# Performance work log

Measured on AMD Instinct MI355X. Metric: run time of the kernel, lower is better.

## Reference

```python
import jax, jax.numpy as jnp
import numpy as np

B, S, D = 2, 1024, 2048
H, KVH, HD = 16, 4, 128
HID, E, K = 4096, 8, 2
EPS = 1e-5
NEG = -1e9  # finite stand-in for -inf in the causal mask


def setup_inputs() -> dict:
    key = jax.random.key(0)
    ks = jax.random.split(key, 16)
    sc = 0.02
    x = jax.random.normal(ks[0], (B, S, D), jnp.float32)
    # rotary tables (theta = 10000), as cos/sin instead of complex
    inv_freq = 1.0 / (10000.0 ** (jnp.arange(0, HD, 2, dtype=jnp.float32) / HD))
    t = jnp.arange(S, dtype=jnp.float32)
    fr = jnp.outer(t, inv_freq)  # [S, HD/2]
    freqs_cos, freqs_sin = jnp.cos(fr), jnp.sin(fr)
    positions = jnp.arange(S, dtype=jnp.int32)
    mask = jnp.where(jnp.tril(jnp.ones((S, S), bool)), 0.0, NEG).astype(jnp.float32)
    attn_norm_w = jnp.ones((D,), jnp.float32)
    ffn_norm_w = jnp.ones((D,), jnp.float32)
    wq = jax.random.normal(ks[1], (D, H * HD), jnp.float32) * sc
    wk = jax.random.normal(ks[2], (D, KVH * HD), jnp.float32) * sc
    wv = jax.random.normal(ks[3], (D, KVH * HD), jnp.float32) * sc
    wo = jax.random.normal(ks[4], (H * HD, D), jnp.float32) * sc
    gate_w = jax.random.normal(ks[5], (D, E), jnp.float32) * sc
    w1 = jax.random.normal(ks[6], (E, D, HID), jnp.float32) * sc
    w2 = jax.random.normal(ks[7], (E, HID, D), jnp.float32) * sc
    w3 = jax.random.normal(ks[8], (E, D, HID), jnp.float32) * sc
    return dict(x=x, freqs_cos=freqs_cos, freqs_sin=freqs_sin, positions=positions,
                mask=mask, attn_norm_w=attn_norm_w, ffn_norm_w=ffn_norm_w,
                wq=wq, wk=wk, wv=wv, wo=wo, gate_w=gate_w, w1=w1, w2=w2, w3=w3)


def rmsnorm(x, w):
    xf = x.astype(jnp.float32)
    n = xf * jax.lax.rsqrt(jnp.mean(xf * xf, axis=-1, keepdims=True) + EPS)
    return n.astype(x.dtype) * w


def rope(t, cos, sin):
    # t: [B,S,nh,HD]; interleaved (real, imag) pairs like torch.view_as_complex
    tr = t.reshape(*t.shape[:-1], HD // 2, 2)
    xr, xi = tr[..., 0], tr[..., 1]
    c = cos[None, :, None, :]
    s = sin[None, :, None, :]
    out = jnp.stack([xr * c - xi * s, xr * s + xi * c], axis=-1)
    return out.reshape(t.shape)


def block_fwd(x, freqs_cos, freqs_sin, mask, attn_norm_w, ffn_norm_w,
              wq, wk, wv, wo, gate_w, w1, w2, w3):
    # ---- attention ----
    h = rmsnorm(x, attn_norm_w)
    q = (h @ wq).reshape(B, S, H, HD)
    k = (h @ wk).reshape(B, S, KVH, HD)
    v = (h @ wv).reshape(B, S, KVH, HD)
    q = rope(q, freqs_cos, freqs_sin)
    k = rope(k, freqs_cos, freqs_sin)
    rep = H // KVH
    k = jnp.repeat(k, rep, axis=2)  # [B,S,H,HD]
    v = jnp.repeat(v, rep, axis=2)
    scale = HD ** -0.5
    scores = jnp.einsum('bqhd,bkhd->bhqk', q, k) * scale + mask[None, None]
    probs = jax.nn.softmax(scores.astype(jnp.float32), axis=-1).astype(q.dtype)
    attn = jnp.einsum('bhqk,bkhd->bqhd', probs, v).reshape(B, S, H * HD)
    h1 = x + attn @ wo
    # ---- MoE FFN ----
    t = rmsnorm(h1, ffn_norm_w).reshape(-1, D)  # [T,D]
    logits = t @ gate_w  # [T,E]
    topw, sel = jax.lax.top_k(logits, K)
    topw = jax.nn.softmax(topw.astype(jnp.float32), axis=-1).astype(t.dtype)
    out = jnp.zeros_like(t)
    for i in range(E):
        coef = jnp.sum(jnp.where(sel == i, topw, 0.0), axis=-1, keepdims=True)  # [T,1]
        ff = (jax.nn.silu(t @ w1[i]) * (t @ w3[i])) @ w2[i]
        out = out + coef * ff
    return h1 + out.reshape(B, S, D)


def reference(x, freqs_cos, freqs_sin, positions, mask, attn_norm_w, ffn_norm_w,
              wq, wk, wv, wo, gate_w, w1, w2, w3):
    # prefill branch (positions.shape[0] > 1): KV-cache scatter is a write-only
    # side effect in the original and does not affect this output.
    del positions
    return block_fwd(x, freqs_cos, freqs_sin, mask, attn_norm_w, ffn_norm_w,
                     wq, wk, wv, wo, gate_w, w1, w2, w3)
```

## Files before the change

### kernel.cpp

```cpp
#include <hip/hip_runtime.h>

typedef unsigned short u16;
typedef unsigned int u32;
typedef __bf16 bf16x8 __attribute__((ext_vector_type(8)));
typedef _Float16 f16;
typedef f16 f16x8 __attribute__((ext_vector_type(8)));
typedef float f32x4 __attribute__((ext_vector_type(4)));

#define DEVFN __device__ __forceinline__

constexpr int kB = 2, kS = 1024, kD = 2048, kH = 16, kKVH = 4, kHD = 128;
constexpr int kHID = 4096, kE = 8;
constexpr int kRows = kB * kS;
constexpr int kQKVN = kH*kHD + 2*kKVH*kHD;
constexpr int kSlotsPad = 5120;
constexpr int kMaxTiles = 40;
constexpr float kEps = 1e-5f;
constexpr float kNeg = -1000000000.0f;
constexpr float kScale = 0.08838834764831845f;

DEVFN u16 f2bf(float f) {
  u32 u = __float_as_uint(f);
  return (u16)((u + 0x7fffu + ((u >> 16) & 1u)) >> 16);
}
DEVFN float bf2f(u16 u) { u32 v = ((u32)u) << 16; return __uint_as_float(v); }

DEVFN void split8v(float4 a, float4 b, f16x8& hi, f16x8& lo) {
  float v[8] = {a.x, a.y, a.z, a.w, b.x, b.y, b.z, b.w};
  #pragma unroll
  for (int e = 0; e < 8; ++e) {
    f16 h = (f16)v[e];
    hi[e] = h;
    lo[e] = (f16)(v[e] - (float)h);
  }
}

DEVFN void gll16(const void* g, void* l) {
  __builtin_amdgcn_global_load_lds(
      (const __attribute__((address_space(1))) void*)g,
      (__attribute__((address_space(3))) void*)l, 16, 0, 0);
}

__global__ __launch_bounds__(256) void rms_split_kernel(const float* __restrict__ in,
    const float* __restrict__ w, f16* __restrict__ oh, f16* __restrict__ ol) {
  int row = blockIdx.x, tid = threadIdx.x;
  const float* x = in + (size_t)row * kD;
  float4 v0 = *(const float4*)&x[tid*8];
  float4 v1 = *(const float4*)&x[tid*8+4];
  float ss = v0.x*v0.x+v0.y*v0.y+v0.z*v0.z+v0.w*v0.w
           + v1.x*v1.x+v1.y*v1.y+v1.z*v1.z+v1.w*v1.w;
  #pragma unroll
  for (int off = 32; off; off >>= 1) ss += __shfl_xor(ss, off);
  __shared__ float red[4];
  if ((tid & 63) == 0) red[tid >> 6] = ss;
  __syncthreads();
  float tot = red[0] + red[1] + red[2] + red[3];
  float rs = rsqrtf(tot * (1.0f/kD) + kEps);
  float4 w0 = *(const float4*)&w[tid*8];
  float4 w1 = *(const float4*)&w[tid*8+4];
  float4 o0, o1;
  o0.x = v0.x*rs*w0.x; o0.y = v0.y*rs*w0.y; o0.z = v0.z*rs*w0.z; o0.w = v0.w*rs*w0.w;
  o1.x = v1.x*rs*w1.x; o1.y = v1.y*rs*w1.y; o1.z = v1.z*rs*w1.z; o1.w = v1.w*rs*w1.w;
  f16x8 hi, lo;
  split8v(o0, o1, hi, lo);
  *(f16x8*)&oh[(size_t)row*kD + tid*8] = hi;
  *(f16x8*)&ol[(size_t)row*kD + tid*8] = lo;
}

__global__ __launch_bounds__(256) void split_kernel(const float* __restrict__ in,
    f16* __restrict__ oh, f16* __restrict__ ol, int n8) {
  int i = blockIdx.x * 256 + threadIdx.x;
  if (i >= n8) return;
  float4 a = *(const float4*)&in[i*8];
  float4 b = *(const float4*)&in[i*8+4];
  f16x8 hi, lo;
  split8v(a, b, hi, lo);
  *(f16x8*)&oh[i*8] = hi;
  *(f16x8*)&ol[i*8] = lo;
}

__global__ __launch_bounds__(256) void rms_bf16_kernel(const float* __restrict__ in,
    const float* __restrict__ w, u16* __restrict__ out) {
  int row = blockIdx.x, tid = threadIdx.x;
  const float* x = in + (size_t)row * kD;
  float4 v0 = *(const float4*)&x[tid*8];
  float4 v1 = *(const float4*)&x[tid*8+4];
  float ss = v0.x*v0.x+v0.y*v0.y+v0.z*v0.z+v0.w*v0.w
           + v1.x*v1.x+v1.y*v1.y+v1.z*v1.z+v1.w*v1.w;
  #pragma unroll
  for (int off = 32; off; off >>= 1) ss += __shfl_xor(ss, off);
  __shared__ float red[4];
  if ((tid & 63) == 0) red[tid >> 6] = ss;
  __syncthreads();
  float tot = red[0] + red[1] + red[2] + red[3];
  float rs = rsqrtf(tot * (1.0f/kD) + kEps);
  float4 w0 = *(const float4*)&w[tid*8];
  float4 w1 = *(const float4*)&w[tid*8+4];
  union { int4 i4; u16 u[8]; } pk;
  pk.u[0] = f2bf(v0.x*rs*w0.x); pk.u[1] = f2bf(v0.y*rs*w0.y);
  pk.u[2] = f2bf(v0.z*rs*w0.z); pk.u[3] = f2bf(v0.w*rs*w0.w);
  pk.u[4] = f2bf(v1.x*rs*w1.x); pk.u[5] = f2bf(v1.y*rs*w1.y);
  pk.u[6] = f2bf(v1.z*rs*w1.z); pk.u[7] = f2bf(v1.w*rs*w1.w);
  *(int4*)&out[(size_t)row*kD + tid*8] = pk.i4;
}

__global__ void transpose_split_kernel(const float* __restrict__ in,
    f16* __restrict__ hi, f16* __restrict__ lo, int R, int C, int noff, int ldout) {
  __shared__ float tile[32][33];
  int c0 = blockIdx.x * 32, r0 = blockIdx.y * 32;
  int tx = threadIdx.x, ty = threadIdx.y;
  #pragma unroll
  for (int i = 0; i < 32; i += 8)
    tile[ty + i][tx] = in[(size_t)(r0 + ty + i) * C + c0 + tx];
  __syncthreads();
  #pragma unroll
  for (int i = 0; i < 32; i += 8) {
    float v = tile[tx][ty + i];
    f16 h = (f16)v;
    size_t o = (size_t)(noff + c0 + ty + i) * ldout + r0 + tx;
    hi[o] = h;
    lo[o] = (f16)(v - (float)h);
  }
}

__global__ __launch_bounds__(256) void transpose_up_kernel(const float* __restrict__ w,
    u16* __restrict__ wUT, int half) {
  int e = blockIdx.z;
  const float* in = w + (size_t)e * kD * kHID;
  u16* out = wUT + (size_t)e * 8192 * kD;
  __shared__ float tile[64][69];
  int c0 = blockIdx.x * 64, r0 = blockIdx.y * 64;
  int tx = threadIdx.x & 15, ty = threadIdx.x >> 4;
  #pragma unroll
  for (int i = 0; i < 4; ++i) {
    float4 v = *(const float4*)&in[(size_t)(r0 + ty + i*16) * kHID + c0 + tx*4];
    tile[ty + i*16][tx*4+0] = v.x;
    tile[ty + i*16][tx*4+1] = v.y;
    tile[ty + i*16][tx*4+2] = v.z;
    tile[ty + i*16][tx*4+3] = v.w;
  }
  __syncthreads();
  int grp = c0 >> 6;
  #pragma unroll
  for (int i = 0; i < 4; ++i) {
    int cl = ty + i*16;
    int rowOut = grp*128 + cl + half*64;
    ushort4 o;
    o.x = f2bf(tile[tx*4+0][cl]);
    o.y = f2bf(tile[tx*4+1][cl]);
    o.z = f2bf(tile[tx*4+2][cl]);
    o.w = f2bf(tile[tx*4+3][cl]);
    *(ushort4*)&out[(size_t)rowOut * kD + r0 + tx*4] = o;
  }
}

__global__ __launch_bounds__(256) void transpose_w2_kernel(const float* __restrict__ w,
    u16* __restrict__ w2T) {
  int e = blockIdx.z;
  const float* in = w + (size_t)e * kHID * kD;
  u16* out = w2T + (size_t)e * kD * kHID;
  __shared__ float tile[64][69];
  int c0 = blockIdx.x * 64, r0 = blockIdx.y * 64;
  int tx = threadIdx.x & 15, ty = threadIdx.x >> 4;
  #pragma unroll
  for (int i = 0; i < 4; ++i) {
    float4 v = *(const float4*)&in[(size_t)(r0 + ty + i*16) * kD + c0 + tx*4];
    tile[ty + i*16][tx*4+0] = v.x;
    tile[ty + i*16][tx*4+1] = v.y;
    tile[ty + i*16][tx*4+2] = v.z;
    tile[ty + i*16][tx*4+3] = v.w;
  }
  __syncthreads();
  #pragma unroll
  for (int i = 0; i < 4; ++i) {
    int cl = ty + i*16;
    ushort4 o;
    o.x = f2bf(tile[tx*4+0][cl]);
    o.y = f2bf(tile[tx*4+1][cl]);
    o.z = f2bf(tile[tx*4+2][cl]);
    o.w = f2bf(tile[tx*4+3][cl]);
    *(ushort4*)&out[(size_t)(c0 + cl) * kHID + r0 + tx*4] = o;
  }
}

__global__ void vt_split_kernel(const float* __restrict__ qkv,
    f16* __restrict__ vTh, f16* __restrict__ vTl) {
  __shared__ float tile[32][33];
  int s0 = blockIdx.x * 32, c0 = blockIdx.y * 32, b = blockIdx.z;
  int tx = threadIdx.x, ty = threadIdx.y;
  #pragma unroll
  for (int i = 0; i < 32; i += 8)
    tile[ty + i][tx] = qkv[(size_t)(b*kS + s0 + ty + i) * kQKVN + kH*kHD + kKVH*kHD + c0 + tx];
  __syncthreads();
  #pragma unroll
  for (int i = 0; i < 32; i += 8) {
    float v = tile[tx][ty + i];
    f16 h = (f16)v;
    size_t o = (size_t)(b*kKVH*kHD + c0 + ty + i) * kS + s0 + tx;
    vTh[o] = h;
    vTl[o] = (f16)(v - (float)h);
  }
}

template<bool ADDX>
__global__ __launch_bounds__(256) void gemm_sf16_kernel(
    const f16* __restrict__ Ah0, const f16* __restrict__ Al0, int lda,
    const f16* __restrict__ Bh0, const f16* __restrict__ Bl0,
    float* __restrict__ C, int ldc, int coff,
    const float* __restrict__ X, int ldx, int K) {
  __shared__ __align__(16) u16 Ah[128*64], Al[128*64], Bh[128*64], Bl[128*64];
  int tid = threadIdx.x, lane = tid & 63, w = tid >> 6;
  int bm = blockIdx.y * 128, bn = blockIdx.x * 128;
  int wr = w >> 1, wc = w & 1;
  int hg = lane >> 4, lid = lane & 15;
  f32x4 acc[4][4] = {};
  const f16 *aH[4], *aL[4], *bH[4], *bL[4];
  #pragma unroll
  for (int j = 0; j < 4; ++j) {
    int r = w*32 + j*8 + (lane >> 3);
    int colc = ((lane & 7) ^ (r & 7)) * 8;
    aH[j] = Ah0 + (size_t)(bm + r) * lda + colc;
    aL[j] = Al0 + (size_t)(bm + r) * lda + colc;
    bH[j] = Bh0 + (size_t)(bn + r) * K + colc;
    bL[j] = Bl0 + (size_t)(bn + r) * K + colc;
  }
  const char* AhB = (const char*)Ah; const char* AlB = (const char*)Al;
  const char* BhB = (const char*)Bh; const char* BlB = (const char*)Bl;
  for (int kt = 0; kt < K; kt += 64) {
    __syncthreads();
    #pragma unroll
    for (int j = 0; j < 4; ++j) {
      int lb = w*2048 + j*512;
      gll16(aH[j] + kt, &Ah[lb]);
      gll16(aL[j] + kt, &Al[lb]);
      gll16(bH[j] + kt, &Bh[lb]);
      gll16(bL[j] + kt, &Bl[lb]);
    }
    __syncthreads();
    #pragma unroll
    for (int kk = 0; kk < 2; ++kk) {
      f16x8 ah[4], al[4], bh[4], bl[4];
      #pragma unroll
      for (int f = 0; f < 4; ++f) {
        int rA = wr*64 + f*16 + lid;
        int oA = (rA*128 + kk*64 + hg*16) ^ ((rA & 7) << 4);
        ah[f] = *(const f16x8*)(AhB + oA);
        al[f] = *(const f16x8*)(AlB + oA);
        int rB = wc*64 + f*16 + lid;
        int oB = (rB*128 + kk*64 + hg*16) ^ ((rB & 7) << 4);
        bh[f] = *(const f16x8*)(BhB + oB);
        bl[f] = *(const f16x8*)(BlB + oB);
      }
      #pragma unroll
      for (int i = 0; i < 4; ++i)
        #pragma unroll
        for (int j = 0; j < 4; ++j) {
          acc[i][j] = __builtin_amdgcn_mfma_f32_16x16x32_f16(ah[i], bh[j], acc[i][j], 0, 0, 0);
          acc[i][j] = __builtin_amdgcn_mfma_f32_16x16x32_f16(ah[i], bl[j], acc[i][j], 0, 0, 0);
          acc[i][j] = __builtin_amdgcn_mfma_f32_16x16x32_f16(al[i], bh[j], acc[i][j], 0, 0, 0);
        }
    }
  }
  #pragma unroll
  for (int i = 0; i < 4; ++i) {
    #pragma unroll
    for (int rr = 0; rr < 4; ++rr) {
      size_t gr = (size_t)(bm + wr*64 + i*16 + hg*4 + rr);
      #pragma unroll
      for (int j = 0; j < 4; ++j) {
        int gc = bn + wc*64 + j*16 + lid;
        float v = acc[i][j][rr];
        if (ADDX) v += X[gr * ldx + gc];
        C[gr * ldc + coff + gc] = v;
      }
    }
  }
}

__global__ __launch_bounds__(256) void rope_kernel(float* __restrict__ qkv,
    const float* __restrict__ fc, const float* __restrict__ fs,
    f16* __restrict__ Kh, f16* __restrict__ Kl) {
  int idx = blockIdx.x * 256 + threadIdx.x;
  constexpr int NQ = kB*kS*kH*(kHD/2);
  constexpr int NK = kB*kS*kKVH*(kHD/2);
  if (idx < NQ) {
    int i = idx & 63, h = (idx >> 6) & 15, s = (idx >> 10) & 1023, b = idx >> 20;
    size_t base = ((size_t)(b*kS + s))*kQKVN + h*kHD + 2*i;
    float c = fc[s*64 + i], sn = fs[s*64 + i];
    float xr = qkv[base], xi = qkv[base+1];
    qkv[base]   = xr*c - xi*sn;
    qkv[base+1] = xr*sn + xi*c;
  } else {
    int j = idx - NQ; if (j >= NK) return;
    int i = j & 63, h = (j >> 6) & 3, s = (j >> 8) & 1023, b = j >> 18;
    size_t src = ((size_t)(b*kS + s))*kQKVN + kH*kHD + h*kHD + 2*i;
    float c = fc[s*64 + i], sn = fs[s*64 + i];
    float xr = qkv[src], xi = qkv[src+1];
    float o0 = xr*c - xi*sn, o1 = xr*sn + xi*c;
    size_t dst = (((size_t)(b*kKVH + h))*kS + s)*kHD + 2*i;
    f16 h0 = (f16)o0, h1 = (f16)o1;
    Kh[dst]   = h0; Kl[dst]   = (f16)(o0 - (float)h0);
    Kh[dst+1] = h1; Kl[dst+1] = (f16)(o1 - (float)h1);
  }
}

__global__ __launch_bounds__(256) void attn_sf16_kernel(const float* __restrict__ qkv,
    const f16* __restrict__ Ksh, const f16* __restrict__ Ksl,
    const f16* __restrict__ vTh, const f16* __restrict__ vTl,
    float* __restrict__ out) {
  int qt = (int)gridDim.x - 1 - blockIdx.x;
  int h = blockIdx.y, b = blockIdx.z;
  int kvh = h >> 2;
  int q0 = qt * 64;
  __shared__ __align__(16) char Kh[64*128*2], Kl[64*128*2];
  __shared__ __align__(16) char Vh[128*64*2], Vl[128*64*2];
  __shared__ __align__(16) char Ph[4][16*64*2], Pl[4][16*64*2];
  int tid = threadIdx.x, lane = tid & 63, w = tid >> 6;
  int hg = lane >> 4, lid = lane & 15;

  f16x8 qh[4], ql[4];
  {
    const float* qrow = qkv + (size_t)(b*kS + q0 + w*16 + lid) * kQKVN + h*kHD;
    #pragma unroll
    for (int ks = 0; ks < 4; ++ks) {
      float4 a = *(const float4*)(qrow + ks*32 + hg*8);
      float4 c = *(const float4*)(qrow + ks*32 + hg*8 + 4);
      split8v(a, c, qh[ks], ql[ks]);
    }
  }
  f32x4 oacc[8] = {};
  float m[4] = {-3.0e38f, -3.0e38f, -3.0e38f, -3.0e38f};
  float lsum[4] = {};
  char* Phw = Ph[w];
  char* Plw = Pl[w];

  for (int kt = 0; kt <= qt; ++kt) {
    __syncthreads();
    {
      int r = tid >> 2, c0 = (tid & 3) * 32;
      const f16* khr = Ksh + ((size_t)(b*kKVH + kvh)*kS + kt*64 + r) * kHD + c0;
      const f16* klr = Ksl + ((size_t)(b*kKVH + kvh)*kS + kt*64 + r) * kHD + c0;
      #pragma unroll
      for (int s8 = 0; s8 < 4; ++s8) {
        int4 hi = *(const int4*)(khr + s8*8);
        int4 lo = *(const int4*)(klr + s8*8);
        int off = (r*256 + c0*2 + s8*16) ^ ((r & 7) << 4);
        *(int4*)(Kh + off) = hi;
        *(int4*)(Kl + off) = lo;
      }
    }
    {
      int r = tid >> 1, c0 = (tid & 1) * 32;
      const f16* vhr = vTh + (size_t)(b*kKVH*kHD + kvh*kHD + r) * kS + kt*64 + c0;
      const f16* vlr = vTl + (size_t)(b*kKVH*kHD + kvh*kHD + r) * kS + kt*64 + c0;
      #pragma unroll
      for (int s8 = 0; s8 < 4; ++s8) {
        int4 hi = *(const int4*)(vhr + s8*8);
        int4 lo = *(const int4*)(vlr + s8*8);
        int off = (r*128 + c0*2 + s8*16) ^ ((r & 7) << 4);
        *(int4*)(Vh + off) = hi;
        *(int4*)(Vl + off) = lo;
      }
    }
    __syncthreads();

    f32x4 sacc[4] = {};
    #pragma unroll
    for (int ks = 0; ks < 4; ++ks) {
      #pragma unroll
      for (int j = 0; j < 4; ++j) {
        int rB = j*16 + lid;
        int off = (rB*256 + ks*64 + hg*16) ^ ((rB & 7) << 4);
        f16x8 kh = *(const f16x8*)(Kh + off);
        f16x8 klo = *(const f16x8*)(Kl + off);
        sacc[j] = __builtin_amdgcn_mfma_f32_16x16x32_f16(qh[ks], kh, sacc[j], 0, 0, 0);
        sacc[j] = __builtin_amdgcn_mfma_f32_16x16x32_f16(qh[ks], klo, sacc[j], 0, 0, 0);
        sacc[j] = __builtin_amdgcn_mfma_f32_16x16x32_f16(ql[ks], kh, sacc[j], 0, 0, 0);
      }
    }
    float s[4][4], ps[4][4];
    bool diag = (kt == qt);
    #pragma unroll
    for (int j = 0; j < 4; ++j)
      #pragma unroll
      for (int r = 0; r < 4; ++r) {
        float v = sacc[j][r] * kScale;
        if (diag) {
          int kvabs = kt*64 + j*16 + lid;
          int qabs = q0 + w*16 + hg*4 + r;
          if (kvabs > qabs) v = kNeg;
        }
        s[j][r] = v;
      }
    float pm[4], cf[4];
    #pragma unroll
    for (int r = 0; r < 4; ++r) {
      pm[r] = fmaxf(fmaxf(s[0][r], s[1][r]), fmaxf(s[2][r], s[3][r]));
      #pragma unroll
      for (int msk = 1; msk < 16; msk <<= 1) pm[r] = fmaxf(pm[r], __shfl_xor(pm[r], msk));
      float mn = fmaxf(m[r], pm[r]);
      cf[r] = __expf(m[r] - mn);
      m[r] = mn;
    }
    #pragma unroll
    for (int j2 = 0; j2 < 8; ++j2)
      #pragma unroll
      for (int r = 0; r < 4; ++r) oacc[j2][r] *= cf[r];
    float rs[4] = {};
    #pragma unroll
    for (int j = 0; j < 4; ++j)
      #pragma unroll
      for (int r = 0; r < 4; ++r) {
        float p = __expf(s[j][r] - m[r]);
        ps[j][r] = p;
        rs[r] += p;
      }
    #pragma unroll
    for (int r = 0; r < 4; ++r) lsum[r] = lsum[r]*cf[r] + rs[r];
    #pragma unroll
    for (int j = 0; j < 4; ++j)
      #pragma unroll
      for (int r = 0; r < 4; ++r) {
        int q = hg*4 + r;
        int off = (q*128 + (j*16 + lid)*2) ^ ((q & 7) << 4);
        f16 ph = (f16)ps[j][r];
        *(f16*)(Phw + off) = ph;
        *(f16*)(Plw + off) = (f16)(ps[j][r] - (float)ph);
      }
    #pragma unroll
    for (int kk2 = 0; kk2 < 2; ++kk2) {
      int oP = (lid*128 + kk2*64 + hg*16) ^ ((lid & 7) << 4);
      f16x8 pa_h = *(const f16x8*)(Phw + oP);
      f16x8 pa_l = *(const f16x8*)(Plw + oP);
      #pragma unroll
      for (int j2 = 0; j2 < 8; ++j2) {
        int rV = j2*16 + lid;
        int off = (rV*128 + kk2*64 + hg*16) ^ ((rV & 7) << 4);
        f16x8 vh = *(const f16x8*)(Vh + off);
        f16x8 vl = *(const f16x8*)(Vl + off);
        oacc[j2] = __builtin_amdgcn_mfma_f32_16x16x32_f16(pa_h, vh, oacc[j2], 0, 0, 0);
        oacc[j2] = __builtin_amdgcn_mfma_f32_16x16x32_f16(pa_h, vl, oacc[j2], 0, 0, 0);
        oacc[j2] = __builtin_amdgcn_mfma_f32_16x16x32_f16(pa_l, vh, oacc[j2], 0, 0, 0);
      }
    }
  }
  #pragma unroll
  for (int r = 0; r < 4; ++r) {
    #pragma unroll
    for (int msk = 1; msk < 16; msk <<= 1) lsum[r] += __shfl_xor(lsum[r], msk);
    lsum[r] = 1.f / lsum[r];
  }
  #pragma unroll
  for (int j2 = 0; j2 < 8; ++j2)
    #pragma unroll
    for (int r = 0; r < 4; ++r) {
      size_t o = (size_t)(b*kS + q0 + w*16 + hg*4 + r) * kD + h*kHD + j2*16 + lid;
      out[o] = oacc[j2][r] * lsum[r];
    }
}

__global__ void zero_counts_kernel(int* counts) {
  if (threadIdx.x < kE) counts[threadIdx.x] = 0;
}

__global__ __launch_bounds__(64) void gate_kernel(const float* __restrict__ h1,
    const float* __restrict__ wn, const float* __restrict__ gw,
    int* __restrict__ packA, int* __restrict__ packB,
    float* __restrict__ cA, float* __restrict__ cB,
    int* __restrict__ lists, int* __restrict__ counts) {
  int row = blockIdx.x, lane = threadIdx.x;
  const float* x = h1 + (size_t)row * kD;
  float ss = 0.f;
  for (int d = lane; d < kD; d += 64) { float v = x[d]; ss = fmaf(v, v, ss); }
  #pragma unroll
  for (int off = 32; off; off >>= 1) ss += __shfl_xor(ss, off);
  float rs = rsqrtf(ss * (1.0f/kD) + kEps);
  float acc[kE] = {};
  for (int d = lane; d < kD; d += 64) {
    float g = x[d] * rs * wn[d];
    const float* gr = gw + (size_t)d * kE;
    #pragma unroll
    for (int e = 0; e < kE; ++e) acc[e] = fmaf(g, gr[e], acc[e]);
  }
  #pragma unroll
  for (int e = 0; e < kE; ++e)
    #pragma unroll
    for (int off = 32; off; off >>= 1) acc[e] += __shfl_xor(acc[e], off);
  if (lane == 0) {
    int i1 = 0; float l1 = acc[0];
    #pragma unroll
    for (int e = 1; e < kE; ++e) if (acc[e] > l1) { l1 = acc[e]; i1 = e; }
    int i2 = -1; float l2 = -3.4e38f;
    #pragma unroll
    for (int e = 0; e < kE; ++e) if (e != i1 && acc[e] > l2) { l2 = acc[e]; i2 = e; }
    float e2 = __expf(l2 - l1);
    float inv = 1.f / (1.f + e2);
    int p1 = atomicAdd(&counts[i1], 1); lists[i1*kRows + p1] = row;
    int p2 = atomicAdd(&counts[i2], 1); lists[i2*kRows + p2] = row;
    packA[row] = i1*2048 + p1; cA[row] = inv;
    packB[row] = i2*2048 + p2; cB[row] = e2 * inv;
  }
}

__global__ void prefix_kernel(const int* __restrict__ counts,
    int* __restrict__ padbase, int* __restrict__ tileTab) {
  if (threadIdx.x == 0) {
    int base = 0, idx = 0;
    for (int e = 0; e < kE; ++e) {
      padbase[e] = base;
      int nt = (counts[e] + 127) >> 7;
      for (int t = 0; t < nt; ++t) tileTab[idx++] = (e << 8) | t;
      base += nt << 7;
    }
    for (; idx < kMaxTiles; ++idx) tileTab[idx] = -1;
  }
}

__global__ __launch_bounds__(256) void gemm_up_kernel(
    const u16* __restrict__ A, const u16* __restrict__ WUT,
    u16* __restrict__ hid, const int* __restrict__ lists,
    const int* __restrict__ counts, const int* __restrict__ padbase,
    const int* __restrict__ tileTab) {
  int tab = tileTab[blockIdx.y];
  if (tab < 0) return;
  int e = tab >> 8, mb = tab & 255;
  int cnt = counts[e];
  int bm = mb * 128;
  int slot0 = padbase[e] + bm;
  const int* ids = lists + e * kRows;
  int g = blockIdx.x;
  const u16* Bt = WUT + (size_t)e * 8192 * kD + (size_t)g * 128 * kD;
  __shared__ __align__(16) u16 SM[32768];
  u16* As = SM;
  u16* Bs = SM + 16384;
  int tid = threadIdx.x, lane = tid & 63, w = tid >> 6;
  int wr = w >> 1, wc = w & 1;
  int hg = lane >> 4, lid = lane & 15;
  f32x4 acc[4][4] = {};
  const u16 *aP[4], *bP[4];
  #pragma unroll
  for (int j = 0; j < 4; ++j) {
    int r = w*32 + j*8 + (lane >> 3);
    int colc = ((lane & 7) ^ (r & 7)) * 8;
    int rr = bm + r; if (rr >= cnt) rr = cnt - 1;
    aP[j] = A + (size_t)ids[rr] * kD + colc;
    bP[j] = Bt + (size_t)r * kD + colc;
  }
  #pragma unroll
  for (int j = 0; j < 4; ++j) {
    int lb = w*2048 + j*512;
    gll16(aP[j], &As[lb]);
    gll16(bP[j], &Bs[lb]);
  }
  __syncthreads();
  for (int t = 0; t < 32; ++t) {
    int cur = t & 1;
    if (t + 1 < 32) {
      int kt = (t + 1) * 64;
      int nb = (cur ^ 1) * 8192;
      #pragma unroll
      for (int j = 0; j < 4; ++j) {
        int lb = nb + w*2048 + j*512;
        gll16(aP[j] + kt, &As[lb]);
        gll16(bP[j] + kt, &Bs[lb]);
      }
    }
    const char* AsB = (const char*)(As + cur*8192);
    const char* BsB = (const char*)(Bs + cur*8192);
    #pragma unroll
    for (int kk = 0; kk < 2; ++kk) {
      bf16x8 af[4], bfv[4];
      #pragma unroll
      for (int f = 0; f < 4; ++f) {
        int rA = wr*64 + f*16 + lid;
        af[f] = *(const bf16x8*)(AsB + ((rA*128 + kk*64 + hg*16) ^ ((rA & 7) << 4)));
        int rB = wc*64 + f*16 + lid;
        bfv[f] = *(const bf16x8*)(BsB + ((rB*128 + kk*64 + hg*16) ^ ((rB & 7) << 4)));
      }
      #pragma unroll
      for (int i = 0; i < 4; ++i)
        #pragma unroll
        for (int j = 0; j < 4; ++j)
          acc[i][j] = __builtin_amdgcn_mfma_f32_16x16x32_bf16(af[i], bfv[j], acc[i][j], 0, 0, 0);
    }
    __syncthreads();
  }
  float* Xch = (float*)SM;
  if (wc == 0) {
    #pragma unroll
    for (int i = 0; i < 4; ++i)
      #pragma unroll
      for (int rr = 0; rr < 4; ++rr) {
        int row = wr*64 + i*16 + hg*4 + rr;
        #pragma unroll
        for (int j = 0; j < 4; ++j)
          Xch[row*64 + j*16 + lid] = acc[i][j][rr];
      }
  }
  __syncthreads();
  if (wc == 1) {
    #pragma unroll
    for (int i = 0; i < 4; ++i)
      #pragma unroll
      for (int rr = 0; rr < 4; ++rr) {
        int row = wr*64 + i*16 + hg*4 + rr;
        u16* orow = hid + (size_t)(slot0 + row) * kHID + g*64;
        #pragma unroll
        for (int j = 0; j < 4; ++j) {
          int col = j*16 + lid;
          float g1 = Xch[row*64 + col];
          float g3 = acc[i][j][rr];
          orow[col] = f2bf(g1 / (1.f + __expf(-g1)) * g3);
        }
      }
  }
}

__global__ __launch_bounds__(256) void gemm_down_kernel(
    const u16* __restrict__ hid, const u16* __restrict__ W2T,
    u16* __restrict__ ff, const int* __restrict__ padbase,
    const int* __restrict__ tileTab) {
  int tab = tileTab[blockIdx.y];
  if (tab < 0) return;
  int e = tab >> 8, mb = tab & 255;
  int slot0 = padbase[e] + mb * 128;
  const u16* Bt = W2T + (size_t)e * kD * kHID;
  int bn = blockIdx.x * 128;
  __shared__ __align__(16) u16 SM[32768];
  u16* As = SM;
  u16* Bs = SM + 16384;
  int tid = threadIdx.x, lane = tid & 63, w = tid >> 6;
  int wr = w >> 1, wc = w & 1;
  int hg = lane >> 4, lid = lane & 15;
  f32x4 acc[4][4] = {};
  const u16 *aP[4], *bP[4];
  #pragma unroll
  for (int j = 0; j < 4; ++j) {
    int r = w*32 + j*8 + (lane >> 3);
    int colc = ((lane & 7) ^ (r & 7)) * 8;
    aP[j] = hid + (size_t)(slot0 + r) * kHID + colc;
    bP[j] = Bt + (size_t)(bn + r) * kHID + colc;
  }
  #pragma unroll
  for (int j = 0; j < 4; ++j) {
    int lb = w*2048 + j*512;
    gll16(aP[j], &As[lb]);
    gll16(bP[j], &Bs[lb]);
  }
  __syncthreads();
  for (int t = 0; t < 64; ++t) {
    int cur = t & 1;
    if (t + 1 < 64) {
      int kt = (t + 1) * 64;
      int nb = (cur ^ 1) * 8192;
      #pragma unroll
      for (int j = 0; j < 4; ++j) {
        int lb = nb + w*2048 + j*512;
        gll16(aP[j] + kt, &As[lb]);
        gll16(bP[j] + kt, &Bs[lb]);
      }
    }
    const char* AsB = (const char*)(As + cur*8192);
    const char* BsB = (const char*)(Bs + cur*8192);
    #pragma unroll
    for (int kk = 0; kk < 2; ++kk) {
      bf16x8 af[4], bfv[4];
      #pragma unroll
      for (int f = 0; f < 4; ++f) {
        int rA = wr*64 + f*16 + lid;
        af[f] = *(const bf16x8*)(AsB + ((rA*128 + kk*64 + hg*16) ^ ((rA & 7) << 4)));
        int rB = wc*64 + f*16 + lid;
        bfv[f] = *(const bf16x8*)(BsB + ((rB*128 + kk*64 + hg*16) ^ ((rB & 7) << 4)));
      }
      #pragma unroll
      for (int i = 0; i < 4; ++i)
        #pragma unroll
        for (int j = 0; j < 4; ++j)
          acc[i][j] = __builtin_amdgcn_mfma_f32_16x16x32_bf16(af[i], bfv[j], acc[i][j], 0, 0, 0);
    }
    __syncthreads();
  }
  #pragma unroll
  for (int i = 0; i < 4; ++i)
    #pragma unroll
    for (int rr = 0; rr < 4; ++rr) {
      int row = wr*64 + i*16 + hg*4 + rr;
      u16* orow = ff + (size_t)(slot0 + row) * kD + bn;
      #pragma unroll
      for (int j = 0; j < 4; ++j)
        orow[wc*64 + j*16 + lid] = f2bf(acc[i][j][rr]);
    }
}

__global__ __launch_bounds__(256) void moe_combine_kernel(
    const u16* __restrict__ ff, const int* __restrict__ padbase,
    const int* __restrict__ packA, const int* __restrict__ packB,
    const float* __restrict__ cA, const float* __restrict__ cB,
    float* __restrict__ outp) {
  int row = blockIdx.x, tid = threadIdx.x;
  int pa = packA[row], pb = packB[row];
  int sa = padbase[pa >> 11] + (pa & 2047);
  int sb = padbase[pb >> 11] + (pb & 2047);
  float ca = cA[row], cb = cB[row];
  union { int4 i4; u16 u[8]; } va, vb;
  va.i4 = *(const int4*)(ff + (size_t)sa * kD + tid*8);
  vb.i4 = *(const int4*)(ff + (size_t)sb * kD + tid*8);
  float* o = outp + (size_t)row * kD + tid*8;
  float4 o0 = *(const float4*)o;
  float4 o1 = *(const float4*)(o + 4);
  o0.x += ca*bf2f(va.u[0]) + cb*bf2f(vb.u[0]);
  o0.y += ca*bf2f(va.u[1]) + cb*bf2f(vb.u[1]);
  o0.z += ca*bf2f(va.u[2]) + cb*bf2f(vb.u[2]);
  o0.w += ca*bf2f(va.u[3]) + cb*bf2f(vb.u[3]);
  o1.x += ca*bf2f(va.u[4]) + cb*bf2f(vb.u[4]);
  o1.y += ca*bf2f(va.u[5]) + cb*bf2f(vb.u[5]);
  o1.z += ca*bf2f(va.u[6]) + cb*bf2f(vb.u[6]);
  o1.w += ca*bf2f(va.u[7]) + cb*bf2f(vb.u[7]);
  *(float4*)o = o0;
  *(float4*)(o + 4) = o1;
}

extern "C" void kernel_launch(void* const* d_in, const int* in_sizes, int n_in,
                              void* d_out, int out_size, void* d_ws, size_t ws_size,
                              hipStream_t stream) {
  const float* x    = (const float*)d_in[0];
  const float* fcos = (const float*)d_in[1];
  const float* fsin = (const float*)d_in[2];
  const float* anw  = (const float*)d_in[5];
  const float* fnw  = (const float*)d_in[6];
  const float* wq   = (const float*)d_in[7];
  const float* wk   = (const float*)d_in[8];
  const float* wv   = (const float*)d_in[9];
  const float* wo   = (const float*)d_in[10];
  const float* gw   = (const float*)d_in[11];
  const float* w1   = (const float*)d_in[12];
  const float* w2   = (const float*)d_in[13];
  const float* w3   = (const float*)d_in[14];
  float* outp = (float*)d_out;

  char* ws = (char*)d_ws;
  size_t off = 0;
  auto alloc = [&](size_t bytes) -> void* {
    void* p = ws + off; off += (bytes + 255) & ~(size_t)255; return p;
  };
  f16* h16h   = (f16*)alloc((size_t)kRows*kD*2);
  f16* h16l   = (f16*)alloc((size_t)kRows*kD*2);
  float* qkv  = (float*)alloc((size_t)kRows*kQKVN*4);
  f16* Ksh    = (f16*)alloc((size_t)kB*kKVH*kS*kHD*2);
  f16* Ksl    = (f16*)alloc((size_t)kB*kKVH*kS*kHD*2);
  f16* vTh    = (f16*)alloc((size_t)kB*kKVH*kHD*kS*2);
  f16* vTl    = (f16*)alloc((size_t)kB*kKVH*kHD*kS*2);
  float* attno= (float*)alloc((size_t)kRows*kD*4);
  f16* a16h   = (f16*)alloc((size_t)kRows*kD*2);
  f16* a16l   = (f16*)alloc((size_t)kRows*kD*2);
  u16* tbf    = (u16*)alloc((size_t)kRows*kD*2);
  int* packA  = (int*)alloc(kRows*4);
  int* packB  = (int*)alloc(kRows*4);
  float* cAv  = (float*)alloc(kRows*4);
  float* cBv  = (float*)alloc(kRows*4);
  int* counts = (int*)alloc(kE*4);
  int* padbase= (int*)alloc(kE*4);
  int* tileTab= (int*)alloc(kMaxTiles*4);
  int* lists  = (int*)alloc((size_t)kE*kRows*4);
  f16* Bqh    = (f16*)alloc((size_t)kQKVN*kD*2);
  f16* Bql    = (f16*)alloc((size_t)kQKVN*kD*2);
  f16* Bwh    = (f16*)alloc((size_t)kD*kD*2);
  f16* Bwl    = (f16*)alloc((size_t)kD*kD*2);
  u16* hid    = (u16*)alloc((size_t)kSlotsPad*kHID*2);
  u16* ffb    = (u16*)alloc((size_t)kSlotsPad*kD*2);
  u16* wUT    = (u16*)alloc((size_t)kE*8192*kD*2);
  u16* w2T    = (u16*)alloc((size_t)kE*kD*kHID*2);

  transpose_split_kernel<<<dim3(kD/32, kD/32), dim3(32,8), 0, stream>>>(wq, Bqh, Bql, kD, 2048, 0, kD);
  transpose_split_kernel<<<dim3(512/32, kD/32), dim3(32,8), 0, stream>>>(wk, Bqh, Bql, kD, 512, 2048, kD);
  transpose_split_kernel<<<dim3(512/32, kD/32), dim3(32,8), 0, stream>>>(wv, Bqh, Bql, kD, 512, 2560, kD);
  transpose_split_kernel<<<dim3(kD/32, kD/32), dim3(32,8), 0, stream>>>(wo, Bwh, Bwl, kD, kD, 0, kD);
  transpose_up_kernel<<<dim3(kHID/64, kD/64, kE), 256, 0, stream>>>(w1, wUT, 0);
  transpose_up_kernel<<<dim3(kHID/64, kD/64, kE), 256, 0, stream>>>(w3, wUT, 1);
  transpose_w2_kernel<<<dim3(kD/64, kHID/64, kE), 256, 0, stream>>>(w2, w2T);

  rms_split_kernel<<<kRows, 256, 0, stream>>>(x, anw, h16h, h16l);
  gemm_sf16_kernel<false><<<dim3(kQKVN/128, kRows/128), 256, 0, stream>>>(
      h16h, h16l, kD, Bqh, Bql, qkv, kQKVN, 0, nullptr, 0, kD);
  rope_kernel<<<(kB*kS*(kH+kKVH)*(kHD/2))/256, 256, 0, stream>>>(qkv, fcos, fsin, Ksh, Ksl);
  vt_split_kernel<<<dim3(kS/32, (kKVH*kHD)/32, kB), dim3(32,8), 0, stream>>>(qkv, vTh, vTl);
  attn_sf16_kernel<<<dim3(kS/64, kH, kB), 256, 0, stream>>>(qkv, Ksh, Ksl, vTh, vTl, attno);
  split_kernel<<<(kRows*kD/8 + 255)/256, 256, 0, stream>>>(attno, a16h, a16l, kRows*kD/8);
  gemm_sf16_kernel<true><<<dim3(kD/128, kRows/128), 256, 0, stream>>>(
      a16h, a16l, kD, Bwh, Bwl, outp, kD, 0, x, kD, kD);

  zero_counts_kernel<<<1, 64, 0, stream>>>(counts);
  gate_kernel<<<kRows, 64, 0, stream>>>(outp, fnw, gw, packA, packB, cAv, cBv, lists, counts);
  prefix_kernel<<<1, 64, 0, stream>>>(counts, padbase, tileTab);
  rms_bf16_kernel<<<kRows, 256, 0, stream>>>(outp, fnw, tbf);

  gemm_up_kernel<<<dim3(64, kMaxTiles), 256, 0, stream>>>(
      tbf, wUT, hid, lists, counts, padbase, tileTab);
  gemm_down_kernel<<<dim3(kD/128, kMaxTiles), 256, 0, stream>>>(
      hid, w2T, ffb, padbase, tileTab);
  moe_combine_kernel<<<kRows, 256, 0, stream>>>(
      ffb, padbase, packA, packB, cAv, cBv, outp);
}
```

Before: 992.3 us.

## Fuse expert weight transpose and bf16 conversion into MoE GEMM loads

Removes the separate transpose/convert kernels for w1, w3 and w2. The MoE up and down GEMMs now read fp32 weights directly through registers, pack them to bf16 and write them into swizzled LDS, with a software-pipelined double buffer. This saves one full read-modify-write pass over the large expert weights. In exchange, each tile re-reads fp32 weights (twice the bytes of bf16) with strided scalar loads, and the rows of each expert are reused across up to several M-tiles. The grid order is swapped so tiles of the same weight column run adjacently, and padded rows are skipped on store.

```diff
diff --git a/kernel.cpp b/kernel.cpp
--- a/kernel.cpp
+++ b/kernel.cpp
@@ -6,6 +6,7 @@
 typedef _Float16 f16;
 typedef f16 f16x8 __attribute__((ext_vector_type(8)));
 typedef float f32x4 __attribute__((ext_vector_type(4)));
+typedef u32 u32x2 __attribute__((ext_vector_type(2)));
 
 #define DEVFN __device__ __forceinline__
 
@@ -39,6 +40,13 @@
   __builtin_amdgcn_global_load_lds(
       (const __attribute__((address_space(1))) void*)g,
       (__attribute__((address_space(3))) void*)l, 16, 0, 0);
+}
+
+DEVFN u32x2 pk4bf(float a, float b, float c, float d) {
+  union { __bf16 h[4]; u32x2 w; } u;
+  u.h[0] = (__bf16)a; u.h[1] = (__bf16)b;
+  u.h[2] = (__bf16)c; u.h[3] = (__bf16)d;
+  return u.w;
 }
 
 __global__ __launch_bounds__(256) void rms_split_kernel(const float* __restrict__ in,
@@ -120,66 +128,6 @@
     size_t o = (size_t)(noff + c0 + ty + i) * ldout + r0 + tx;
     hi[o] = h;
     lo[o] = (f16)(v - (float)h);
-  }
-}
-
-__global__ __launch_bounds__(256) void transpose_up_kernel(const float* __restrict__ w,
-    u16* __restrict__ wUT, int half) {
-  int e = blockIdx.z;
-  const float* in = w + (size_t)e * kD * kHID;
-  u16* out = wUT + (size_t)e * 8192 * kD;
-  __shared__ float tile[64][69];
-  int c0 = blockIdx.x * 64, r0 = blockIdx.y * 64;
-  int tx = threadIdx.x & 15, ty = threadIdx.x >> 4;
-  #pragma unroll
-  for (int i = 0; i < 4; ++i) {
-    float4 v = *(const float4*)&in[(size_t)(r0 + ty + i*16) * kHID + c0 + tx*4];
-    tile[ty + i*16][tx*4+0] = v.x;
-    tile[ty + i*16][tx*4+1] = v.y;
-    tile[ty + i*16][tx*4+2] = v.z;
-    tile[ty + i*16][tx*4+3] = v.w;
-  }
-  __syncthreads();
-  int grp = c0 >> 6;
-  #pragma unroll
-  for (int i = 0; i < 4; ++i) {
-    int cl = ty + i*16;
-    int rowOut = grp*128 + cl + half*64;
-    ushort4 o;
-    o.x = f2bf(tile[tx*4+0][cl]);
-    o.y = f2bf(tile[tx*4+1][cl]);
-    o.z = f2bf(tile[tx*4+2][cl]);
-    o.w = f2bf(tile[tx*4+3][cl]);
-    *(ushort4*)&out[(size_t)rowOut * kD + r0 + tx*4] = o;
-  }
-}
-
-__global__ __launch_bounds__(256) void transpose_w2_kernel(const float* __restrict__ w,
-    u16* __restrict__ w2T) {
-  int e = blockIdx.z;
-  const float* in = w + (size_t)e * kHID * kD;
-  u16* out = w2T + (size_t)e * kD * kHID;
-  __shared__ float tile[64][69];
-  int c0 = blockIdx.x * 64, r0 = blockIdx.y * 64;
-  int tx = threadIdx.x & 15, ty = threadIdx.x >> 4;
-  #pragma unroll
-  for (int i = 0; i < 4; ++i) {
-    float4 v = *(const float4*)&in[(size_t)(r0 + ty + i*16) * kD + c0 + tx*4];
-    tile[ty + i*16][tx*4+0] = v.x;
-    tile[ty + i*16][tx*4+1] = v.y;
-    tile[ty + i*16][tx*4+2] = v.z;
-    tile[ty + i*16][tx*4+3] = v.w;
-  }
-  __syncthreads();
-  #pragma unroll
-  for (int i = 0; i < 4; ++i) {
-    int cl = ty + i*16;
-    ushort4 o;
-    o.x = f2bf(tile[tx*4+0][cl]);
-    o.y = f2bf(tile[tx*4+1][cl]);
-    o.z = f2bf(tile[tx*4+2][cl]);
-    o.w = f2bf(tile[tx*4+3][cl]);
-    *(ushort4*)&out[(size_t)(c0 + cl) * kHID + r0 + tx*4] = o;
   }
 }
 
@@ -517,56 +465,69 @@
 }
 
 __global__ __launch_bounds__(256) void gemm_up_kernel(
-    const u16* __restrict__ A, const u16* __restrict__ WUT,
+    const u16* __restrict__ A, const float* __restrict__ W1, const float* __restrict__ W3,
     u16* __restrict__ hid, const int* __restrict__ lists,
     const int* __restrict__ counts, const int* __restrict__ padbase,
     const int* __restrict__ tileTab) {
-  int tab = tileTab[blockIdx.y];
+  int tab = tileTab[blockIdx.x];
   if (tab < 0) return;
   int e = tab >> 8, mb = tab & 255;
   int cnt = counts[e];
   int bm = mb * 128;
   int slot0 = padbase[e] + bm;
   const int* ids = lists + e * kRows;
-  int g = blockIdx.x;
-  const u16* Bt = WUT + (size_t)e * 8192 * kD + (size_t)g * 128 * kD;
-  __shared__ __align__(16) u16 SM[32768];
-  u16* As = SM;
-  u16* Bs = SM + 16384;
+  int g = blockIdx.y;
+  __shared__ __align__(16) char SM[65536];
+  u16* As[2]   = { (u16*)SM, (u16*)(SM + 16384) };
+  char* B1s[2] = { SM + 32768, SM + 40960 };
+  char* B3s[2] = { SM + 49152, SM + 57344 };
   int tid = threadIdx.x, lane = tid & 63, w = tid >> 6;
   int wr = w >> 1, wc = w & 1;
   int hg = lane >> 4, lid = lane & 15;
   f32x4 acc[4][4] = {};
-  const u16 *aP[4], *bP[4];
+
+  const u16* aP[4];
   #pragma unroll
   for (int j = 0; j < 4; ++j) {
     int r = w*32 + j*8 + (lane >> 3);
     int colc = ((lane & 7) ^ (r & 7)) * 8;
     int rr = bm + r; if (rr >= cnt) rr = cnt - 1;
     aP[j] = A + (size_t)ids[rr] * kD + colc;
-    bP[j] = Bt + (size_t)r * kD + colc;
-  }
-  #pragma unroll
-  for (int j = 0; j < 4; ++j) {
-    int lb = w*2048 + j*512;
-    gll16(aP[j], &As[lb]);
-    gll16(bP[j], &Bs[lb]);
-  }
-  __syncthreads();
-  for (int t = 0; t < 32; ++t) {
-    int cur = t & 1;
-    if (t + 1 < 32) {
-      int kt = (t + 1) * 64;
-      int nb = (cur ^ 1) * 8192;
+  }
+  const float* b1e = W1 + (size_t)e*kD*kHID + (size_t)g*64 + lane;
+  const float* b3e = W3 + (size_t)e*kD*kHID + (size_t)g*64 + lane;
+  int wOff[4];
+  #pragma unroll
+  for (int s = 0; s < 4; ++s)
+    wOff[s] = (lane*128 + s*32 + w*8) ^ ((lane & 7) << 4);
+
+  auto stageA = [&](int buf, int t) {
+    int kt = t * 64;
+    #pragma unroll
+    for (int j = 0; j < 4; ++j) gll16(aP[j] + kt, &As[buf][w*2048 + j*512]);
+  };
+  float r1v[4][4], r3v[4][4];
+  auto loadB = [&](int t) {
+    int kt = t * 64;
+    #pragma unroll
+    for (int s = 0; s < 4; ++s)
       #pragma unroll
       for (int j = 0; j < 4; ++j) {
-        int lb = nb + w*2048 + j*512;
-        gll16(aP[j] + kt, &As[lb]);
-        gll16(bP[j] + kt, &Bs[lb]);
-      }
-    }
-    const char* AsB = (const char*)(As + cur*8192);
-    const char* BsB = (const char*)(Bs + cur*8192);
+        size_t ko = (size_t)(kt + s*16 + w*4 + j) * kHID;
+        r1v[s][j] = b1e[ko];
+        r3v[s][j] = b3e[ko];
+      }
+  };
+  auto writeB = [&](int buf) {
+    #pragma unroll
+    for (int s = 0; s < 4; ++s) {
+      *(u32x2*)(B1s[buf] + wOff[s]) = pk4bf(r1v[s][0], r1v[s][1], r1v[s][2], r1v[s][3]);
+      *(u32x2*)(B3s[buf] + wOff[s]) = pk4bf(r3v[s][0], r3v[s][1], r3v[s][2], r3v[s][3]);
+    }
+  };
+  auto compute = [&](int buf) {
+    const char* AsB = (const char*)As[buf];
+    const char* Bb = wc ? B3s[buf] : B1s[buf];
     #pragma unroll
     for (int kk = 0; kk < 2; ++kk) {
       bf16x8 af[4], bfv[4];
@@ -574,8 +535,8 @@
       for (int f = 0; f < 4; ++f) {
         int rA = wr*64 + f*16 + lid;
         af[f] = *(const bf16x8*)(AsB + ((rA*128 + kk*64 + hg*16) ^ ((rA & 7) << 4)));
-        int rB = wc*64 + f*16 + lid;
-        bfv[f] = *(const bf16x8*)(BsB + ((rB*128 + kk*64 + hg*16) ^ ((rB & 7) << 4)));
+        int rB = f*16 + lid;
+        bfv[f] = *(const bf16x8*)(Bb + ((rB*128 + kk*64 + hg*16) ^ ((rB & 7) << 4)));
       }
       #pragma unroll
       for (int i = 0; i < 4; ++i)
@@ -583,8 +544,24 @@
         for (int j = 0; j < 4; ++j)
           acc[i][j] = __builtin_amdgcn_mfma_f32_16x16x32_bf16(af[i], bfv[j], acc[i][j], 0, 0, 0);
     }
+  };
+
+  constexpr int NT = kD / 64;
+  stageA(0, 0);
+  loadB(0);
+  writeB(0);
+  __syncthreads();
+  for (int t = 0; t < NT; t += 2) {
+    stageA(1, t+1); loadB(t+1);
+    compute(0);
+    writeB(1);
     __syncthreads();
-  }
+    if (t+2 < NT) { stageA(0, t+2); loadB(t+2); }
+    compute(1);
+    if (t+2 < NT) writeB(0);
+    __syncthreads();
+  }
+
   float* Xch = (float*)SM;
   if (wc == 0) {
     #pragma unroll
@@ -604,6 +581,8 @@
       #pragma unroll
       for (int rr = 0; rr < 4; ++rr) {
         int row = wr*64 + i*16 + hg*4 + rr;
+        int gr = bm + row;
+        if (gr >= cnt) continue;
         u16* orow = hid + (size_t)(slot0 + row) * kHID + g*64;
         #pragma unroll
         for (int j = 0; j < 4; ++j) {
@@ -617,51 +596,59 @@
 }
 
 __global__ __launch_bounds__(256) void gemm_down_kernel(
-    const u16* __restrict__ hid, const u16* __restrict__ W2T,
+    const u16* __restrict__ hid, const float* __restrict__ W2,
     u16* __restrict__ ff, const int* __restrict__ padbase,
     const int* __restrict__ tileTab) {
-  int tab = tileTab[blockIdx.y];
+  int tab = tileTab[blockIdx.x];
   if (tab < 0) return;
   int e = tab >> 8, mb = tab & 255;
   int slot0 = padbase[e] + mb * 128;
-  const u16* Bt = W2T + (size_t)e * kD * kHID;
-  int bn = blockIdx.x * 128;
-  __shared__ __align__(16) u16 SM[32768];
-  u16* As = SM;
-  u16* Bs = SM + 16384;
+  int bn = blockIdx.y * 128;
+  __shared__ __align__(16) char SM[65536];
+  u16* As[2] = { (u16*)SM, (u16*)(SM + 16384) };
+  char* Bs[2] = { SM + 32768, SM + 49152 };
   int tid = threadIdx.x, lane = tid & 63, w = tid >> 6;
   int wr = w >> 1, wc = w & 1;
   int hg = lane >> 4, lid = lane & 15;
   f32x4 acc[4][4] = {};
-  const u16 *aP[4], *bP[4];
+
+  const u16* aP[4];
   #pragma unroll
   for (int j = 0; j < 4; ++j) {
     int r = w*32 + j*8 + (lane >> 3);
     int colc = ((lane & 7) ^ (r & 7)) * 8;
     aP[j] = hid + (size_t)(slot0 + r) * kHID + colc;
-    bP[j] = Bt + (size_t)(bn + r) * kHID + colc;
-  }
-  #pragma unroll
-  for (int j = 0; j < 4; ++j) {
-    int lb = w*2048 + j*512;
-    gll16(aP[j], &As[lb]);
-    gll16(bP[j], &Bs[lb]);
-  }
-  __syncthreads();
-  for (int t = 0; t < 64; ++t) {
-    int cur = t & 1;
-    if (t + 1 < 64) {
-      int kt = (t + 1) * 64;
-      int nb = (cur ^ 1) * 8192;
-      #pragma unroll
-      for (int j = 0; j < 4; ++j) {
-        int lb = nb + w*2048 + j*512;
-        gll16(aP[j] + kt, &As[lb]);
-        gll16(bP[j] + kt, &Bs[lb]);
-      }
-    }
-    const char* AsB = (const char*)(As + cur*8192);
-    const char* BsB = (const char*)(Bs + cur*8192);
+  }
+  int nrow = (w & 1)*64 + lane;
+  int kq = w >> 1;
+  const float* b2e = W2 + (size_t)e*kHID*kD + (size_t)bn + nrow;
+  int wOff[8];
+  #pragma unroll
+  for (int s = 0; s < 8; ++s)
+    wOff[s] = (nrow*128 + s*16 + kq*8) ^ ((nrow & 7) << 4);
+
+  auto stageA = [&](int buf, int t) {
+    int kt = t * 64;
+    #pragma unroll
+    for (int j = 0; j < 4; ++j) gll16(aP[j] + kt, &As[buf][w*2048 + j*512]);
+  };
+  float rbv[8][4];
+  auto loadB = [&](int t) {
+    int kt = t * 64;
+    #pragma unroll
+    for (int s = 0; s < 8; ++s)
+      #pragma unroll
+      for (int j = 0; j < 4; ++j)
+        rbv[s][j] = b2e[(size_t)(kt + s*8 + kq*4 + j) * kD];
+  };
+  auto writeB = [&](int buf) {
+    #pragma unroll
+    for (int s = 0; s < 8; ++s)
+      *(u32x2*)(Bs[buf] + wOff[s]) = pk4bf(rbv[s][0], rbv[s][1], rbv[s][2], rbv[s][3]);
+  };
+  auto compute = [&](int buf) {
+    const char* AsB = (const char*)As[buf];
+    const char* Bb = Bs[buf];
     #pragma unroll
     for (int kk = 0; kk < 2; ++kk) {
       bf16x8 af[4], bfv[4];
@@ -670,7 +657,7 @@
         int rA = wr*64 + f*16 + lid;
         af[f] = *(const bf16x8*)(AsB + ((rA*128 + kk*64 + hg*16) ^ ((rA & 7) << 4)));
         int rB = wc*64 + f*16 + lid;
-        bfv[f] = *(const bf16x8*)(BsB + ((rB*128 + kk*64 + hg*16) ^ ((rB & 7) << 4)));
+        bfv[f] = *(const bf16x8*)(Bb + ((rB*128 + kk*64 + hg*16) ^ ((rB & 7) << 4)));
       }
       #pragma unroll
       for (int i = 0; i < 4; ++i)
@@ -678,8 +665,24 @@
         for (int j = 0; j < 4; ++j)
           acc[i][j] = __builtin_amdgcn_mfma_f32_16x16x32_bf16(af[i], bfv[j], acc[i][j], 0, 0, 0);
     }
+  };
+
+  constexpr int NT = kHID / 64;
+  stageA(0, 0);
+  loadB(0);
+  writeB(0);
+  __syncthreads();
+  for (int t = 0; t < NT; t += 2) {
+    stageA(1, t+1); loadB(t+1);
+    compute(0);
+    writeB(1);
     __syncthreads();
-  }
+    if (t+2 < NT) { stageA(0, t+2); loadB(t+2); }
+    compute(1);
+    if (t+2 < NT) writeB(0);
+    __syncthreads();
+  }
+
   #pragma unroll
   for (int i = 0; i < 4; ++i)
     #pragma unroll
@@ -768,16 +771,11 @@
   f16* Bwl    = (f16*)alloc((size_t)kD*kD*2);
   u16* hid    = (u16*)alloc((size_t)kSlotsPad*kHID*2);
   u16* ffb    = (u16*)alloc((size_t)kSlotsPad*kD*2);
-  u16* wUT    = (u16*)alloc((size_t)kE*8192*kD*2);
-  u16* w2T    = (u16*)alloc((size_t)kE*kD*kHID*2);
 
   transpose_split_kernel<<<dim3(kD/32, kD/32), dim3(32,8), 0, stream>>>(wq, Bqh, Bql, kD, 2048, 0, kD);
   transpose_split_kernel<<<dim3(512/32, kD/32), dim3(32,8), 0, stream>>>(wk, Bqh, Bql, kD, 512, 2048, kD);
   transpose_split_kernel<<<dim3(512/32, kD/32), dim3(32,8), 0, stream>>>(wv, Bqh, Bql, kD, 512, 2560, kD);
   transpose_split_kernel<<<dim3(kD/32, kD/32), dim3(32,8), 0, stream>>>(wo, Bwh, Bwl, kD, kD, 0, kD);
-  transpose_up_kernel<<<dim3(kHID/64, kD/64, kE), 256, 0, stream>>>(w1, wUT, 0);
-  transpose_up_kernel<<<dim3(kHID/64, kD/64, kE), 256, 0, stream>>>(w3, wUT, 1);
-  transpose_w2_kernel<<<dim3(kD/64, kHID/64, kE), 256, 0, stream>>>(w2, w2T);
 
   rms_split_kernel<<<kRows, 256, 0, stream>>>(x, anw, h16h, h16l);
   gemm_sf16_kernel<false><<<dim3(kQKVN/128, kRows/128), 256, 0, stream>>>(
@@ -794,10 +792,10 @@
   prefix_kernel<<<1, 64, 0, stream>>>(counts, padbase, tileTab);
   rms_bf16_kernel<<<kRows, 256, 0, stream>>>(outp, fnw, tbf);
 
-  gemm_up_kernel<<<dim3(64, kMaxTiles), 256, 0, stream>>>(
-      tbf, wUT, hid, lists, counts, padbase, tileTab);
-  gemm_down_kernel<<<dim3(kD/128, kMaxTiles), 256, 0, stream>>>(
-      hid, w2T, ffb, padbase, tileTab);
+  gemm_up_kernel<<<dim3(kMaxTiles, kHID/64), 256, 0, stream>>>(
+      tbf, w1, w3, hid, lists, counts, padbase, tileTab);
+  gemm_down_kernel<<<dim3(kMaxTiles, kD/128), 256, 0, stream>>>(
+      hid, w2, ffb, padbase, tileTab);
   moe_combine_kernel<<<kRows, 256, 0, stream>>>(
       ffb, padbase, packA, packB, cAv, cBv, outp);
 }
```

Result: slower. 1.101 ms (+10.9%).
